# Kernel optimization log

Measured on AMD Instinct MI355X. Metric: run time of the kernel, lower is better.

The kernel has to match this reference:

```python
import jax, jax.numpy as jnp
import numpy as np


def _conv(x, w, b):
    # x: [B,C,H,W], w: [O,I,3,3] -> SAME conv
    y = jax.lax.conv_general_dilated(x, w, window_strides=(1, 1), padding='SAME',
                                     dimension_numbers=('NCHW', 'OIHW', 'NCHW'))
    return y + b[None, :, None, None]


def _ode_f(y, W1, b1, W2, b2):
    # neural ODE vector field f(t, y) (autonomous conv net)
    return _conv(jnp.tanh(_conv(y, W1, b1)), W2, b2)


def setup_inputs() -> dict:
    key = jax.random.key(0)
    k0, k1, k2 = jax.random.split(key, 3)
    B, C, H, W, T = 16, 128, 32, 32, 25
    first_point = jax.random.normal(k0, (B, C, H, W), dtype=jnp.float32)
    # integration grid over [0, 0.96], one RK4 step per interval (torchdiffeq 'rk4')
    time_steps_to_predict = jnp.arange(T, dtype=jnp.float32) * 0.04
    W1 = jax.random.normal(k1, (C, C, 3, 3), dtype=jnp.float32) * 0.05
    b1 = jnp.zeros((C,), dtype=jnp.float32)
    W2 = jax.random.normal(k2, (C, C, 3, 3), dtype=jnp.float32) * 0.05
    b2 = jnp.zeros((C,), dtype=jnp.float32)
    return {'first_point': first_point, 'time_steps_to_predict': time_steps_to_predict,
            'W1': W1, 'b1': b1, 'W2': W2, 'b2': b2}


def reference(first_point, time_steps_to_predict, W1, b1, W2, b2):
    # DiffeqSolver.forward (nru=nru2=False): pred = odeint(f, y0, t) with fixed-grid RK4
    # (one step per consecutive time pair), then permute [T,B,C,H,W] -> [B,T,C,H,W].
    f = lambda y: _ode_f(y, W1, b1, W2, b2)

    def rk4_step(y, dt):
        k1 = f(y)
        k2 = f(y + 0.5 * dt * k1)
        k3 = f(y + 0.5 * dt * k2)
        k4 = f(y + dt * k3)
        y1 = y + (dt / 6.0) * (k1 + 2.0 * k2 + 2.0 * k3 + k4)
        return y1, y1

    dts = jnp.diff(time_steps_to_predict)           # [T-1]
    _, ys = jax.lax.scan(rk4_step, first_point, dts)  # [T-1,B,C,H,W]
    pred = jnp.concatenate([first_point[None], ys], axis=0)  # [T,B,C,H,W]
    return jnp.transpose(pred, (1, 0, 2, 3, 4))     # [B,T,C,H,W]
```

## Files before the change

kernel.cpp:

```cpp
#include <hip/hip_runtime.h>
#include <hip/hip_bf16.h>
#include <math.h>

typedef __attribute__((ext_vector_type(8))) short bf16x8;
typedef __attribute__((ext_vector_type(4))) float f32x4;
typedef __attribute__((ext_vector_type(4))) unsigned short u16x4;

#define B_   16
#define C_   128
#define CHW_ 131072

__device__ __forceinline__ unsigned short f2bf(float f) {
  union { float f; unsigned int i; } v; v.f = f;
  unsigned int lsb = (v.i >> 16) & 1u;
  v.i += 0x7fffu + lsb;
  return (unsigned short)(v.i >> 16);
}

__global__ void prep_weights(const float* __restrict__ W1, const float* __restrict__ W2,
                             unsigned short* __restrict__ w1bf, unsigned short* __restrict__ w2bf) {
  int j = blockIdx.x * 256 + threadIdx.x;
  if (j >= 2 * 147456) return;
  int which = j / 147456;
  int r = j - which * 147456;
  int ks = r >> 12;
  int co = (r >> 5) & 127;
  int c5 = r & 31;
  int off = ks >> 2;
  int ci  = (ks & 3) * 32 + c5;
  const float* src = which ? W2 : W1;
  unsigned short* dst = which ? w2bf : w1bf;
  dst[r] = f2bf(src[(co * 128 + ci) * 9 + off]);
}

__global__ void init_copy(const float* __restrict__ y0, float* __restrict__ y32,
                          float* __restrict__ dout) {
  int i = blockIdx.x * 256 + threadIdx.x;
  if (i >= B_ * CHW_) return;
  float v = y0[i];
  y32[i] = v;
  int b = i >> 17, chw = i & (CHW_ - 1);
  dout[b * 25 * CHW_ + chw] = v;
}

__global__ void init_transpose(const float* __restrict__ y0, unsigned short* __restrict__ tmp_bf) {
  __shared__ float t[32][33];
  int blk = blockIdx.x;
  int b = blk >> 7;
  int rem = blk & 127;
  int co0 = (rem >> 5) * 32;
  int p0  = (rem & 31) * 32;
  int tx = threadIdx.x & 31, ty = threadIdx.x >> 5;
  #pragma unroll
  for (int k = 0; k < 4; k++) {
    int cl = ty + k * 8;
    t[cl][tx] = y0[b * CHW_ + (co0 + cl) * 1024 + p0 + tx];
  }
  __syncthreads();
  #pragma unroll
  for (int k = 0; k < 4; k++) {
    int pl = ty + k * 8;
    tmp_bf[(b * 1024 + p0 + pl) * 128 + co0 + tx] = f2bf(t[tx][pl]);
  }
}

template<int ST>
__global__ __launch_bounds__(512, 1)
void fused_stage(const unsigned short* __restrict__ w1bf,
                 const unsigned short* __restrict__ w2bf,
                 const float* __restrict__ b1v, const float* __restrict__ b2v,
                 unsigned short* __restrict__ tmp_bf,
                 float* __restrict__ y32, float* __restrict__ acc32,
                 float* __restrict__ dout, const float* __restrict__ tarr, int step)
{
  __shared__ unsigned short IT[204 * 136];
  __shared__ unsigned short ZT[136 * 136];
  const int tid  = threadIdx.x;
  const int img  = blockIdx.x >> 4;
  const int r0   = (blockIdx.x & 15) * 2;
  const int lane = tid & 63;
  const int wave = tid >> 6;
  const int lhi  = lane >> 4;
  const int llo  = lane & 15;

  const unsigned short* a1base = w1bf + (wave * 16 + llo) * 32 + lhi * 8;
  const unsigned short* a2base = w2bf + (wave * 16 + llo) * 32 + lhi * 8;

  float t0 = tarr[step];
  float t1 = tarr[step + 1];
  asm volatile("" : "+v"(t1));
  const float dt = t1 - t0;
  const float dt6 = dt * (1.f / 6.f), dt3 = dt * (1.f / 3.f), dth = dt * 0.5f;

  for (int chunk = tid; chunk < 204 * 16 + 128; chunk += 512) {
    if (chunk < 204 * 16) {
      int pix = chunk >> 4;
      int oct = chunk & 15;
      int ir = pix / 34, ic = pix - ir * 34;
      int gr = r0 - 2 + ir, gc = ic - 1;
      bf16x8 v = {0, 0, 0, 0, 0, 0, 0, 0};
      if ((unsigned)gr < 32u && (unsigned)gc < 32u)
        v = *(const bf16x8*)(tmp_bf + ((img * 32 + gr) * 32 + gc) * 128 + oct * 8);
      *(bf16x8*)(IT + pix * 136 + oct * 8) = v;
    } else {
      int padidx = chunk - 204 * 16;
      int zp  = padidx >> 4;
      int oct = padidx & 15;
      int zpix = (zp >> 1) * 34 + ((zp & 1) ? 33 : 0);
      bf16x8 z = {0, 0, 0, 0, 0, 0, 0, 0};
      *(bf16x8*)(ZT + zpix * 136 + oct * 8) = z;
    }
  }
  __syncthreads();

  {
    f32x4 a1[4][2];
    #pragma unroll
    for (int i = 0; i < 4; i++) { a1[i][0] = (f32x4){0,0,0,0}; a1[i][1] = (f32x4){0,0,0,0}; }
    #pragma unroll
    for (int dw = 0; dw < 3; ++dw) {
      #pragma unroll
      for (int kk = 0; kk < 4; ++kk) {
        bf16x8 bfr[6][2];
        #pragma unroll
        for (int rr = 0; rr < 6; ++rr) {
          const int prow = rr * 34 + llo + dw;
          bfr[rr][0] = *(const bf16x8*)(IT + prow * 136 + kk * 32 + lhi * 8);
          bfr[rr][1] = *(const bf16x8*)(IT + (prow + 16) * 136 + kk * 32 + lhi * 8);
        }
        bf16x8 afr[3];
        #pragma unroll
        for (int dh = 0; dh < 3; ++dh)
          afr[dh] = *(const bf16x8*)(a1base + ((dh * 3 + dw) * 4 + kk) * 4096);
        #pragma unroll
        for (int dh = 0; dh < 3; ++dh)
          #pragma unroll
          for (int zr = 0; zr < 4; ++zr)
            #pragma unroll
            for (int spt = 0; spt < 2; ++spt)
              a1[zr][spt] = __builtin_amdgcn_mfma_f32_16x16x32_bf16(afr[dh], bfr[zr + dh][spt], a1[zr][spt], 0, 0, 0);
      }
    }
    const int co = wave * 16 + lhi * 4;
    f32x4 bia = *(const f32x4*)(b1v + co);
    #pragma unroll
    for (int zr = 0; zr < 4; ++zr) {
      const bool live = (unsigned)(r0 - 1 + zr) < 32u;
      #pragma unroll
      for (int spt = 0; spt < 2; ++spt) {
        const int c = spt * 16 + llo;
        u16x4 pk;
        #pragma unroll
        for (int reg = 0; reg < 4; ++reg)
          pk[reg] = live ? f2bf(tanhf(a1[zr][spt][reg] + bia[reg])) : (unsigned short)0;
        *(u16x4*)(ZT + (zr * 34 + c + 1) * 136 + co) = pk;
      }
    }
  }
  __syncthreads();

  {
    f32x4 a2[2][2];
    #pragma unroll
    for (int i = 0; i < 2; i++) { a2[i][0] = (f32x4){0,0,0,0}; a2[i][1] = (f32x4){0,0,0,0}; }
    #pragma unroll
    for (int dw = 0; dw < 3; ++dw) {
      #pragma unroll
      for (int kk = 0; kk < 4; ++kk) {
        bf16x8 bfr[4][2];
        #pragma unroll
        for (int rr = 0; rr < 4; ++rr) {
          const int zpix = rr * 34 + llo + dw;
          bfr[rr][0] = *(const bf16x8*)(ZT + zpix * 136 + kk * 32 + lhi * 8);
          bfr[rr][1] = *(const bf16x8*)(ZT + (zpix + 16) * 136 + kk * 32 + lhi * 8);
        }
        bf16x8 afr[3];
        #pragma unroll
        for (int dh = 0; dh < 3; ++dh)
          afr[dh] = *(const bf16x8*)(a2base + ((dh * 3 + dw) * 4 + kk) * 4096);
        #pragma unroll
        for (int dh = 0; dh < 3; ++dh)
          #pragma unroll
          for (int q = 0; q < 2; ++q)
            #pragma unroll
            for (int spt = 0; spt < 2; ++spt)
              a2[q][spt] = __builtin_amdgcn_mfma_f32_16x16x32_bf16(afr[dh], bfr[q + dh][spt], a2[q][spt], 0, 0, 0);
      }
    }
    const int co0 = wave * 16 + lhi * 4;
    f32x4 bia = *(const f32x4*)(b2v + co0);
    #pragma unroll
    for (int q = 0; q < 2; ++q) {
      const int row = r0 + q;
      #pragma unroll
      for (int spt = 0; spt < 2; ++spt) {
        const int col = spt * 16 + llo;
        const int pnhwc = (img * 1024 + row * 32 + col) * 128 + co0;
        const int idx0  = img * CHW_ + co0 * 1024 + row * 32 + col;
        u16x4 pk;
        #pragma unroll
        for (int reg = 0; reg < 4; ++reg) {
          float kv = a2[q][spt][reg] + bia[reg];
          int id = idx0 + reg * 1024;
          float tv;
          if constexpr (ST == 1)      { float yv = y32[id]; acc32[id] = yv + dt6 * kv; tv = yv + dth * kv; }
          else if constexpr (ST == 2) { float yv = y32[id]; acc32[id] += dt3 * kv;     tv = yv + dth * kv; }
          else if constexpr (ST == 3) { float yv = y32[id]; acc32[id] += dt3 * kv;     tv = yv + dt * kv; }
          else {
            tv = acc32[id] + dt6 * kv;
            y32[id] = tv;
            dout[(img * 25 + step + 1) * CHW_ + co0 * 1024 + row * 32 + col + reg * 1024] = tv;
          }
          pk[reg] = f2bf(tv);
        }
        *(u16x4*)(tmp_bf + pnhwc) = pk;
      }
    }
  }
}

extern "C" void kernel_launch(void* const* d_in, const int* in_sizes, int n_in,
                              void* d_out, int out_size, void* d_ws, size_t ws_size,
                              hipStream_t stream) {
  const float* y0   = (const float*)d_in[0];
  const float* tarr = (const float*)d_in[1];
  const float* W1   = (const float*)d_in[2];
  const float* b1   = (const float*)d_in[3];
  const float* W2   = (const float*)d_in[4];
  const float* b2   = (const float*)d_in[5];
  float* dout = (float*)d_out;

  char* ws = (char*)d_ws;
  float* y32             = (float*)(ws);
  float* acc32           = (float*)(ws + (8u << 20));
  unsigned short* tmp_bf = (unsigned short*)(ws + (16u << 20));
  unsigned short* w1bf   = (unsigned short*)(ws + (20u << 20));
  unsigned short* w2bf   = (unsigned short*)(ws + (20u << 20) + 294912);

  prep_weights<<<(2 * 147456 + 255) / 256, 256, 0, stream>>>(W1, W2, w1bf, w2bf);
  init_copy<<<(B_ * CHW_ + 255) / 256, 256, 0, stream>>>(y0, y32, dout);
  init_transpose<<<2048, 256, 0, stream>>>(y0, tmp_bf);

  for (int step = 0; step < 24; ++step) {
    fused_stage<1><<<256, 512, 0, stream>>>(w1bf, w2bf, b1, b2, tmp_bf, y32, acc32, dout, tarr, step);
    fused_stage<2><<<256, 512, 0, stream>>>(w1bf, w2bf, b1, b2, tmp_bf, y32, acc32, dout, tarr, step);
    fused_stage<3><<<256, 512, 0, stream>>>(w1bf, w2bf, b1, b2, tmp_bf, y32, acc32, dout, tarr, step);
    fused_stage<4><<<256, 512, 0, stream>>>(w1bf, w2bf, b1, b2, tmp_bf, y32, acc32, dout, tarr, step);
  }
}
```

Before: 2.351 ms.

## Repartition waves over output channels and rows in fused conv stage

Changes the per-wave tiling of both convolutions. Each wave previously owned 16 output channels across all rows; now it owns 32 channels and half the rows (two z-rows in conv1, one output row in conv2). This cuts LDS B-fragment reads per MFMA, since each B fragment is reused across two channel tiles, while A (weight) loads from global memory double per wave. The MFMA count per wave stays the same, but register pressure and the balance between LDS and global traffic shift.

Result: slower. 2.845 ms (+21.0%).

```diff
diff --git a/kernel.cpp b/kernel.cpp
--- a/kernel.cpp
+++ b/kernel.cpp
@@ -83,8 +83,12 @@
   const int lhi  = lane >> 4;
   const int llo  = lane & 15;
 
-  const unsigned short* a1base = w1bf + (wave * 16 + llo) * 32 + lhi * 8;
-  const unsigned short* a2base = w2bf + (wave * 16 + llo) * 32 + lhi * 8;
+  const int ch  = (wave & 3) * 32;
+  const int zrp = (wave >> 2) * 2;
+  const int row_w = wave >> 2;
+
+  const unsigned short* a1base = w1bf + (ch + llo) * 32 + lhi * 8;
+  const unsigned short* a2base = w2bf + (ch + llo) * 32 + lhi * 8;
 
   float t0 = tarr[step];
   float t1 = tarr[step + 1];
@@ -114,84 +118,101 @@
   __syncthreads();
 
   {
-    f32x4 a1[4][2];
-    #pragma unroll
-    for (int i = 0; i < 4; i++) { a1[i][0] = (f32x4){0,0,0,0}; a1[i][1] = (f32x4){0,0,0,0}; }
+    f32x4 a1[2][2][2];
+    #pragma unroll
+    for (int i = 0; i < 2; i++)
+      #pragma unroll
+      for (int j = 0; j < 2; j++) {
+        a1[i][j][0] = (f32x4){0, 0, 0, 0};
+        a1[i][j][1] = (f32x4){0, 0, 0, 0};
+      }
     #pragma unroll
     for (int dw = 0; dw < 3; ++dw) {
       #pragma unroll
       for (int kk = 0; kk < 4; ++kk) {
-        bf16x8 bfr[6][2];
-        #pragma unroll
-        for (int rr = 0; rr < 6; ++rr) {
-          const int prow = rr * 34 + llo + dw;
+        bf16x8 bfr[4][2];
+        #pragma unroll
+        for (int rr = 0; rr < 4; ++rr) {
+          const int prow = (zrp + rr) * 34 + llo + dw;
           bfr[rr][0] = *(const bf16x8*)(IT + prow * 136 + kk * 32 + lhi * 8);
           bfr[rr][1] = *(const bf16x8*)(IT + (prow + 16) * 136 + kk * 32 + lhi * 8);
         }
-        bf16x8 afr[3];
-        #pragma unroll
-        for (int dh = 0; dh < 3; ++dh)
-          afr[dh] = *(const bf16x8*)(a1base + ((dh * 3 + dw) * 4 + kk) * 4096);
+        bf16x8 afr[3][2];
+        #pragma unroll
+        for (int dh = 0; dh < 3; ++dh) {
+          const int ks = (dh * 3 + dw) * 4 + kk;
+          afr[dh][0] = *(const bf16x8*)(a1base + ks * 4096);
+          afr[dh][1] = *(const bf16x8*)(a1base + ks * 4096 + 512);
+        }
         #pragma unroll
         for (int dh = 0; dh < 3; ++dh)
           #pragma unroll
-          for (int zr = 0; zr < 4; ++zr)
+          for (int ct = 0; ct < 2; ++ct)
+            #pragma unroll
+            for (int q = 0; q < 2; ++q)
+              #pragma unroll
+              for (int spt = 0; spt < 2; ++spt)
+                a1[ct][q][spt] = __builtin_amdgcn_mfma_f32_16x16x32_bf16(afr[dh][ct], bfr[q + dh][spt], a1[ct][q][spt], 0, 0, 0);
+      }
+    }
+    #pragma unroll
+    for (int ct = 0; ct < 2; ++ct) {
+      const int co = ch + ct * 16 + lhi * 4;
+      f32x4 bia = *(const f32x4*)(b1v + co);
+      #pragma unroll
+      for (int q = 0; q < 2; ++q) {
+        const int zr = zrp + q;
+        const bool live = (unsigned)(r0 - 1 + zr) < 32u;
+        #pragma unroll
+        for (int spt = 0; spt < 2; ++spt) {
+          const int c = spt * 16 + llo;
+          u16x4 pk;
+          #pragma unroll
+          for (int reg = 0; reg < 4; ++reg)
+            pk[reg] = live ? f2bf(tanhf(a1[ct][q][spt][reg] + bia[reg])) : (unsigned short)0;
+          *(u16x4*)(ZT + (zr * 34 + c + 1) * 136 + co) = pk;
+        }
+      }
+    }
+  }
+  __syncthreads();
+
+  {
+    f32x4 a2[2][2];
+    #pragma unroll
+    for (int i = 0; i < 2; i++) { a2[i][0] = (f32x4){0,0,0,0}; a2[i][1] = (f32x4){0,0,0,0}; }
+    #pragma unroll
+    for (int dw = 0; dw < 3; ++dw) {
+      #pragma unroll
+      for (int kk = 0; kk < 4; ++kk) {
+        bf16x8 bfr[3][2];
+        #pragma unroll
+        for (int dh = 0; dh < 3; ++dh) {
+          const int zpix = (row_w + dh) * 34 + llo + dw;
+          bfr[dh][0] = *(const bf16x8*)(ZT + zpix * 136 + kk * 32 + lhi * 8);
+          bfr[dh][1] = *(const bf16x8*)(ZT + (zpix + 16) * 136 + kk * 32 + lhi * 8);
+        }
+        bf16x8 afr[3][2];
+        #pragma unroll
+        for (int dh = 0; dh < 3; ++dh) {
+          const int ks = (dh * 3 + dw) * 4 + kk;
+          afr[dh][0] = *(const bf16x8*)(a2base + ks * 4096);
+          afr[dh][1] = *(const bf16x8*)(a2base + ks * 4096 + 512);
+        }
+        #pragma unroll
+        for (int dh = 0; dh < 3; ++dh)
+          #pragma unroll
+          for (int ct = 0; ct < 2; ++ct)
             #pragma unroll
             for (int spt = 0; spt < 2; ++spt)
-              a1[zr][spt] = __builtin_amdgcn_mfma_f32_16x16x32_bf16(afr[dh], bfr[zr + dh][spt], a1[zr][spt], 0, 0, 0);
-      }
-    }
-    const int co = wave * 16 + lhi * 4;
-    f32x4 bia = *(const f32x4*)(b1v + co);
-    #pragma unroll
-    for (int zr = 0; zr < 4; ++zr) {
-      const bool live = (unsigned)(r0 - 1 + zr) < 32u;
-      #pragma unroll
-      for (int spt = 0; spt < 2; ++spt) {
-        const int c = spt * 16 + llo;
-        u16x4 pk;
-        #pragma unroll
-        for (int reg = 0; reg < 4; ++reg)
-          pk[reg] = live ? f2bf(tanhf(a1[zr][spt][reg] + bia[reg])) : (unsigned short)0;
-        *(u16x4*)(ZT + (zr * 34 + c + 1) * 136 + co) = pk;
-      }
-    }
-  }
-  __syncthreads();
-
-  {
-    f32x4 a2[2][2];
-    #pragma unroll
-    for (int i = 0; i < 2; i++) { a2[i][0] = (f32x4){0,0,0,0}; a2[i][1] = (f32x4){0,0,0,0}; }
-    #pragma unroll
-    for (int dw = 0; dw < 3; ++dw) {
-      #pragma unroll
-      for (int kk = 0; kk < 4; ++kk) {
-        bf16x8 bfr[4][2];
-        #pragma unroll
-        for (int rr = 0; rr < 4; ++rr) {
-          const int zpix = rr * 34 + llo + dw;
-          bfr[rr][0] = *(const bf16x8*)(ZT + zpix * 136 + kk * 32 + lhi * 8);
-          bfr[rr][1] = *(const bf16x8*)(ZT + (zpix + 16) * 136 + kk * 32 + lhi * 8);
-        }
-        bf16x8 afr[3];
-        #pragma unroll
-        for (int dh = 0; dh < 3; ++dh)
-          afr[dh] = *(const bf16x8*)(a2base + ((dh * 3 + dw) * 4 + kk) * 4096);
-        #pragma unroll
-        for (int dh = 0; dh < 3; ++dh)
-          #pragma unroll
-          for (int q = 0; q < 2; ++q)
-            #pragma unroll
-            for (int spt = 0; spt < 2; ++spt)
-              a2[q][spt] = __builtin_amdgcn_mfma_f32_16x16x32_bf16(afr[dh], bfr[q + dh][spt], a2[q][spt], 0, 0, 0);
-      }
-    }
-    const int co0 = wave * 16 + lhi * 4;
-    f32x4 bia = *(const f32x4*)(b2v + co0);
-    #pragma unroll
-    for (int q = 0; q < 2; ++q) {
-      const int row = r0 + q;
+              a2[ct][spt] = __builtin_amdgcn_mfma_f32_16x16x32_bf16(afr[dh][ct], bfr[dh][spt], a2[ct][spt], 0, 0, 0);
+      }
+    }
+    const int row = r0 + row_w;
+    #pragma unroll
+    for (int ct = 0; ct < 2; ++ct) {
+      const int co0 = ch + ct * 16 + lhi * 4;
+      f32x4 bia = *(const f32x4*)(b2v + co0);
       #pragma unroll
       for (int spt = 0; spt < 2; ++spt) {
         const int col = spt * 16 + llo;
@@ -200,7 +221,7 @@
         u16x4 pk;
         #pragma unroll
         for (int reg = 0; reg < 4; ++reg) {
-          float kv = a2[q][spt][reg] + bia[reg];
+          float kv = a2[ct][spt][reg] + bia[reg];
           int id = idx0 + reg * 1024;
           float tv;
           if constexpr (ST == 1)      { float yv = y32[id]; acc32[id] = yv + dt6 * kv; tv = yv + dth * kv; }
```

## Pad LDS stride, use fast tanh, prefetch RK state before second conv

Applied to the files above, without the earlier changes.

The shared-memory row stride goes from 136 to 138 halfwords so the MFMA fragment reads hit fewer LDS bank conflicts. tanhf is replaced by an exp plus hardware-reciprocal approximation. The y32 and acc32 values for the RK4 epilogue are now loaded into registers before the second convolution's MFMA loop, so their global latency overlaps compute. The prefetch adds up to 32 live registers under launch_bounds(512,1), and the approximate tanh can differ slightly in accuracy.

Result: faster. 2.247 ms (median of 2 runs) (-4.4%).

```diff
diff --git a/kernel.cpp b/kernel.cpp
--- a/kernel.cpp
+++ b/kernel.cpp
@@ -9,12 +9,18 @@
 #define B_   16
 #define C_   128
 #define CHW_ 131072
+#define STR_ 138
 
 __device__ __forceinline__ unsigned short f2bf(float f) {
   union { float f; unsigned int i; } v; v.f = f;
   unsigned int lsb = (v.i >> 16) & 1u;
   v.i += 0x7fffu + lsb;
   return (unsigned short)(v.i >> 16);
+}
+
+__device__ __forceinline__ float fast_tanh(float x) {
+  float e = __expf(2.f * x);
+  return 1.f - 2.f * __builtin_amdgcn_rcpf(e + 1.f);
 }
 
 __global__ void prep_weights(const float* __restrict__ W1, const float* __restrict__ W2,
@@ -73,8 +79,8 @@
                  float* __restrict__ y32, float* __restrict__ acc32,
                  float* __restrict__ dout, const float* __restrict__ tarr, int step)
 {
-  __shared__ unsigned short IT[204 * 136];
-  __shared__ unsigned short ZT[136 * 136];
+  __shared__ unsigned short IT[204 * STR_];
+  __shared__ unsigned short ZT[136 * STR_];
   const int tid  = threadIdx.x;
   const int img  = blockIdx.x >> 4;
   const int r0   = (blockIdx.x & 15) * 2;
@@ -101,19 +107,21 @@
       bf16x8 v = {0, 0, 0, 0, 0, 0, 0, 0};
       if ((unsigned)gr < 32u && (unsigned)gc < 32u)
         v = *(const bf16x8*)(tmp_bf + ((img * 32 + gr) * 32 + gc) * 128 + oct * 8);
-      *(bf16x8*)(IT + pix * 136 + oct * 8) = v;
+      *(bf16x8*)(IT + pix * STR_ + oct * 8) = v;
     } else {
       int padidx = chunk - 204 * 16;
       int zp  = padidx >> 4;
       int oct = padidx & 15;
       int zpix = (zp >> 1) * 34 + ((zp & 1) ? 33 : 0);
       bf16x8 z = {0, 0, 0, 0, 0, 0, 0, 0};
-      *(bf16x8*)(ZT + zpix * 136 + oct * 8) = z;
+      *(bf16x8*)(ZT + zpix * STR_ + oct * 8) = z;
     }
   }
   __syncthreads();
 
   {
+    const int co = wave * 16 + lhi * 4;
+    f32x4 bia = *(const f32x4*)(b1v + co);
     f32x4 a1[4][2];
     #pragma unroll
     for (int i = 0; i < 4; i++) { a1[i][0] = (f32x4){0,0,0,0}; a1[i][1] = (f32x4){0,0,0,0}; }
@@ -125,8 +133,8 @@
         #pragma unroll
         for (int rr = 0; rr < 6; ++rr) {
           const int prow = rr * 34 + llo + dw;
-          bfr[rr][0] = *(const bf16x8*)(IT + prow * 136 + kk * 32 + lhi * 8);
-          bfr[rr][1] = *(const bf16x8*)(IT + (prow + 16) * 136 + kk * 32 + lhi * 8);
+          bfr[rr][0] = *(const bf16x8*)(IT + prow * STR_ + kk * 32 + lhi * 8);
+          bfr[rr][1] = *(const bf16x8*)(IT + (prow + 16) * STR_ + kk * 32 + lhi * 8);
         }
         bf16x8 afr[3];
         #pragma unroll
@@ -141,8 +149,6 @@
               a1[zr][spt] = __builtin_amdgcn_mfma_f32_16x16x32_bf16(afr[dh], bfr[zr + dh][spt], a1[zr][spt], 0, 0, 0);
       }
     }
-    const int co = wave * 16 + lhi * 4;
-    f32x4 bia = *(const f32x4*)(b1v + co);
     #pragma unroll
     for (int zr = 0; zr < 4; ++zr) {
       const bool live = (unsigned)(r0 - 1 + zr) < 32u;
@@ -152,14 +158,29 @@
         u16x4 pk;
         #pragma unroll
         for (int reg = 0; reg < 4; ++reg)
-          pk[reg] = live ? f2bf(tanhf(a1[zr][spt][reg] + bia[reg])) : (unsigned short)0;
-        *(u16x4*)(ZT + (zr * 34 + c + 1) * 136 + co) = pk;
+          pk[reg] = live ? f2bf(fast_tanh(a1[zr][spt][reg] + bia[reg])) : (unsigned short)0;
+        *(u16x4*)(ZT + (zr * 34 + c + 1) * STR_ + co) = pk;
       }
     }
   }
   __syncthreads();
 
   {
+    const int co0 = wave * 16 + lhi * 4;
+    f32x4 bia = *(const f32x4*)(b2v + co0);
+    float ypre[2][2][4], apre[2][2][4];
+    #pragma unroll
+    for (int q = 0; q < 2; ++q)
+      #pragma unroll
+      for (int spt = 0; spt < 2; ++spt) {
+        const int idx0 = img * CHW_ + co0 * 1024 + (r0 + q) * 32 + spt * 16 + llo;
+        #pragma unroll
+        for (int reg = 0; reg < 4; ++reg) {
+          if constexpr (ST <= 3) ypre[q][spt][reg] = y32[idx0 + reg * 1024];
+          if constexpr (ST >= 2) apre[q][spt][reg] = acc32[idx0 + reg * 1024];
+        }
+      }
+
     f32x4 a2[2][2];
     #pragma unroll
     for (int i = 0; i < 2; i++) { a2[i][0] = (f32x4){0,0,0,0}; a2[i][1] = (f32x4){0,0,0,0}; }
@@ -171,8 +192,8 @@
         #pragma unroll
         for (int rr = 0; rr < 4; ++rr) {
           const int zpix = rr * 34 + llo + dw;
-          bfr[rr][0] = *(const bf16x8*)(ZT + zpix * 136 + kk * 32 + lhi * 8);
-          bfr[rr][1] = *(const bf16x8*)(ZT + (zpix + 16) * 136 + kk * 32 + lhi * 8);
+          bfr[rr][0] = *(const bf16x8*)(ZT + zpix * STR_ + kk * 32 + lhi * 8);
+          bfr[rr][1] = *(const bf16x8*)(ZT + (zpix + 16) * STR_ + kk * 32 + lhi * 8);
         }
         bf16x8 afr[3];
         #pragma unroll
@@ -187,8 +208,7 @@
               a2[q][spt] = __builtin_amdgcn_mfma_f32_16x16x32_bf16(afr[dh], bfr[q + dh][spt], a2[q][spt], 0, 0, 0);
       }
     }
-    const int co0 = wave * 16 + lhi * 4;
-    f32x4 bia = *(const f32x4*)(b2v + co0);
+
     #pragma unroll
     for (int q = 0; q < 2; ++q) {
       const int row = r0 + q;
@@ -203,11 +223,11 @@
           float kv = a2[q][spt][reg] + bia[reg];
           int id = idx0 + reg * 1024;
           float tv;
-          if constexpr (ST == 1)      { float yv = y32[id]; acc32[id] = yv + dt6 * kv; tv = yv + dth * kv; }
-          else if constexpr (ST == 2) { float yv = y32[id]; acc32[id] += dt3 * kv;     tv = yv + dth * kv; }
-          else if constexpr (ST == 3) { float yv = y32[id]; acc32[id] += dt3 * kv;     tv = yv + dt * kv; }
+          if constexpr (ST == 1)      { float yv = ypre[q][spt][reg]; acc32[id] = yv + dt6 * kv; tv = yv + dth * kv; }
+          else if constexpr (ST == 2) { float yv = ypre[q][spt][reg]; acc32[id] = apre[q][spt][reg] + dt3 * kv; tv = yv + dth * kv; }
+          else if constexpr (ST == 3) { float yv = ypre[q][spt][reg]; acc32[id] = apre[q][spt][reg] + dt3 * kv; tv = yv + dt * kv; }
           else {
-            tv = acc32[id] + dt6 * kv;
+            tv = apre[q][spt][reg] + dt6 * kv;
             y32[id] = tv;
             dout[(img * 25 + step + 1) * CHW_ + co0 * 1024 + row * 32 + col + reg * 1024] = tv;
           }
```
